# Kernel optimization log

Measured on AMD Instinct MI355X. Metric: run time of the kernel, lower is better.

## Reference

```python
import jax, jax.numpy as jnp
import numpy as np

EPS = 1e-5
NEG_SLOPE = 0.1


def setup_inputs() -> dict:
    key = jax.random.key(0)
    ks = jax.random.split(key, 4)
    B, Cin, Cout, D, E, EMB = 2, 32, 32, 40, 3, 1
    return {
        "x": jax.random.normal(ks[0], (B, Cin, D, D, D), dtype=jnp.float32),
        "embedding": jax.random.normal(ks[1], (B, EMB), dtype=jnp.float32),
        "route_w": jax.random.normal(ks[2], (EMB, E), dtype=jnp.float32),
        "route_b": jnp.zeros((E,), dtype=jnp.float32),
        "expert_kernels": jax.random.normal(ks[3], (E, Cout, Cin, 3, 3, 3), dtype=jnp.float32) * 0.05,
        "expert_bias": jnp.zeros((E, Cout), dtype=jnp.float32),
        "gamma": jnp.ones((Cout,), dtype=jnp.float32),
        "beta": jnp.zeros((Cout,), dtype=jnp.float32),
    }


def reference(x, embedding, route_w, route_b, expert_kernels, expert_bias, gamma, beta):
    # CondConv routing: sigmoid(Linear(embedding)) -> per-sample expert weights [B, E]
    r = jax.nn.sigmoid(embedding @ route_w + route_b)
    # Per-sample combined kernel [B, O, I, 3, 3, 3] and bias [B, O]
    w = jnp.einsum('be,eoixyz->boixyz', r, expert_kernels)
    b = r @ expert_bias

    def conv_one(xi, wi):
        # xi: [Cin, D, H, W], wi: [O, I, 3, 3, 3] -> [Cout, D, H, W]
        return jax.lax.conv_general_dilated(
            xi[None], wi, window_strides=(1, 1, 1), padding='SAME',
            dimension_numbers=('NCDHW', 'OIDHW', 'NCDHW'))[0]

    y = jax.vmap(conv_one)(x, w) + b[:, :, None, None, None]  # [B, O, D, H, W]

    # BatchNorm3d (training mode: biased batch stats over B,D,H,W per channel)
    mean = jnp.mean(y, axis=(0, 2, 3, 4), keepdims=True)
    var = jnp.mean(jnp.square(y - mean), axis=(0, 2, 3, 4), keepdims=True)
    y = (y - mean) * jax.lax.rsqrt(var + EPS)
    y = y * gamma[None, :, None, None, None] + beta[None, :, None, None, None]

    # LeakyReLU(0.1)
    y = jnp.where(y >= 0, y, NEG_SLOPE * y)

    # Upsample nearest, scale_factor=2 on all 3 spatial dims
    y = jnp.repeat(jnp.repeat(jnp.repeat(y, 2, axis=2), 2, axis=3), 2, axis=4)
    return y
```

## Files before the change

### kernel.cpp

```cpp
#include <hip/hip_runtime.h>
#include <hip/hip_bf16.h>
#include <math.h>

#define BB   2
#define CIN  32
#define COUT 32
#define DM   40
#define PD   42
#define NPTS (DM*DM)
#define NVOL (DM*DM*DM)
#define EPSBN 1e-5f
#define NSLOT 64

typedef short  bf16x8  __attribute__((ext_vector_type(8)));
typedef float  floatx4 __attribute__((ext_vector_type(4)));

#define WS_WFRAG 0
#define WS_BCOMB 27648
#define WS_SUM2  27712
#define WS_XPAD2 31808
#define WS_Y     2402624

#define REPACK_BLOCKS (PD*PD*BB)
#define NW_ELEMS  (2*2*27*64*8)
#define PREP_ELEMS (NW_ELEMS + 64 + NSLOT*64)
#define PREP_BLOCKS ((PREP_ELEMS + 255) / 256)

__global__ void prep_repack_kernel(const float* __restrict__ x,
                                   const float* __restrict__ emb,
                                   const float* __restrict__ rw,
                                   const float* __restrict__ rb,
                                   const float* __restrict__ ek,
                                   const float* __restrict__ ebias,
                                   float* __restrict__ ws) {
    const int bid = blockIdx.x;
    if (bid < REPACK_BLOCKS) {
        int b  = bid / (PD * PD);
        int r  = bid % (PD * PD);
        int zp = r / PD, yp = r % PD;
        __hip_bfloat16* row = (__hip_bfloat16*)(ws + WS_XPAD2) +
                              ((((size_t)b * PD + zp) * PD + yp) * PD) * 32;
        bool inz = (zp >= 1 && zp <= DM && yp >= 1 && yp <= DM);
        for (int idx = threadIdx.x; idx < PD * 32; idx += 256) {
            int i = idx & 31, xp = idx >> 5;
            float v = 0.0f;
            if (inz && xp >= 1 && xp <= DM)
                v = x[(size_t)(b * CIN + i) * NVOL +
                      (zp - 1) * NPTS + (yp - 1) * DM + (xp - 1)];
            row[idx] = __float2bfloat16(v);
        }
        return;
    }
    int idx = (bid - REPACK_BLOCKS) * 256 + threadIdx.x;
    __hip_bfloat16* wfrag = (__hip_bfloat16*)(ws + WS_WFRAG);
    if (idx < NW_ELEMS) {
        int j    = idx & 7;
        int lane = (idx >> 3) & 63;
        int tap  = (idx >> 9) % 27;
        int nt   = (idx / (27 * 512)) & 1;
        int b    = idx / (2 * 27 * 512);
        int o = nt * 16 + (lane & 15);
        int i = (lane >> 4) * 8 + j;
        float e0 = emb[b];
        float w = 0.0f;
        #pragma unroll
        for (int e = 0; e < 3; ++e) {
            float r = 1.0f / (1.0f + expf(-(e0 * rw[e] + rb[e])));
            w += r * ek[((e * COUT + o) * CIN + i) * 27 + tap];
        }
        wfrag[idx] = __float2bfloat16(w);
    } else if (idx < NW_ELEMS + 64) {
        int j2 = idx - NW_ELEMS;
        int b = j2 >> 5, o = j2 & 31;
        float e0 = emb[b];
        float bv = 0.0f;
        #pragma unroll
        for (int e = 0; e < 3; ++e) {
            float r = 1.0f / (1.0f + expf(-(e0 * rw[e] + rb[e])));
            bv += r * ebias[e * COUT + o];
        }
        ws[WS_BCOMB + j2] = bv;
    } else if (idx < PREP_ELEMS) {
        ws[WS_SUM2 + (idx - NW_ELEMS - 64)] = 0.0f;
    }
}

__global__ __launch_bounds__(256, 4) void conv_mfma_kernel(
        const __hip_bfloat16* __restrict__ xp2,
        const bf16x8* __restrict__ wfrag,
        const float* __restrict__ bcomb,
        float* __restrict__ y,
        float* __restrict__ sums2) {
    const int mc = blockIdx.x, z = blockIdx.y, b = blockIdx.z;
    const int tid = threadIdx.x, lane = tid & 63, wv = tid >> 6;
    const int mt = wv & 1, nt = wv >> 1;
    const int quad = lane >> 4, l15 = lane & 15;

    __shared__ float lstat[64];
    if (tid < 64) lstat[tid] = 0.0f;
    __syncthreads();

    const int pa = mc * 32 + mt * 16 + l15;
    const int ya = pa / DM, xa = pa % DM;
    const char* abase = (const char*)xp2 +
        ((((size_t)b * PD + z) * PD + ya) * PD + xa) * 64 + quad * 16;
    const bf16x8* wbase = wfrag + ((b * 2 + nt) * 27) * 64 + lane;

    floatx4 acc0 = {0.f, 0.f, 0.f, 0.f};
    floatx4 acc1 = {0.f, 0.f, 0.f, 0.f};
    #pragma unroll
    for (int t = 0; t < 27; ++t) {
        const int dz = t / 9, dy = (t / 3) % 3, dx = t % 3;
        bf16x8 av = *(const bf16x8*)(abase + ((dz * PD + dy) * PD + dx) * 64);
        bf16x8 bv = wbase[t * 64];
        if (t & 1) acc1 = __builtin_amdgcn_mfma_f32_16x16x32_bf16(av, bv, acc1, 0, 0, 0);
        else       acc0 = __builtin_amdgcn_mfma_f32_16x16x32_bf16(av, bv, acc0, 0, 0, 0);
    }
    floatx4 acc = acc0 + acc1;

    const int o = nt * 16 + l15;
    const float bias = bcomb[b * COUT + o];
    const int po = mc * 32 + mt * 16 + quad * 4;
    float v0 = acc[0] + bias;
    float v1 = acc[1] + bias;
    float v2 = acc[2] + bias;
    float v3 = acc[3] + bias;
    *(float4*)(y + ((size_t)(b * COUT + o) * DM + z) * NPTS + po) =
        make_float4(v0, v1, v2, v3);

    float vs = v0 + v1 + v2 + v3;
    float vq = v0 * v0 + v1 * v1 + v2 * v2 + v3 * v3;
    vs += __shfl_xor(vs, 16); vq += __shfl_xor(vq, 16);
    vs += __shfl_xor(vs, 32); vq += __shfl_xor(vq, 32);
    if (lane < 16) {
        atomicAdd(&lstat[o],      vs);
        atomicAdd(&lstat[32 + o], vq);
    }
    __syncthreads();
    if (tid < 64) {
        int slot = ((b * DM + z) * 50 + mc) & (NSLOT - 1);
        atomicAdd(&sums2[slot * 64 + tid], lstat[tid]);
    }
}

__global__ void upsample_kernel(const float* __restrict__ yin,
                                const float* __restrict__ sums2,
                                const float* __restrict__ gamma,
                                const float* __restrict__ beta,
                                float* __restrict__ out) {
    __shared__ float partl[4][64];
    __shared__ float ssc[32], ssh[32];
    const int tid = threadIdx.x;
    {
        int sg = tid >> 6, st = tid & 63;
        float p = 0.0f;
        #pragma unroll
        for (int s = 0; s < 16; ++s) p += sums2[(sg * 16 + s) * 64 + st];
        partl[sg][st] = p;
    }
    __syncthreads();
    if (tid < 64) {
        partl[0][tid] += partl[1][tid] + partl[2][tid] + partl[3][tid];
    }
    __syncthreads();
    if (tid < 32) {
        const float invN = 1.0f / (float)(BB * NVOL);
        float mean  = partl[0][tid] * invN;
        float var   = partl[0][32 + tid] * invN - mean * mean;
        float scale = gamma[tid] * rsqrtf(var + EPSBN);
        ssc[tid] = scale;
        ssh[tid] = beta[tid] - mean * scale;
    }
    __syncthreads();

    int idx = blockIdx.x * 256 + tid;
    int cc = idx / (NVOL / 2);
    int p  = idx % (NVOL / 2);
    int z  = p / (NPTS / 2);
    int yy = (p / (DM / 2)) % DM;
    int x2 = p % (DM / 2);
    int c  = cc & 31;

    float2 v = *(const float2*)(yin + (size_t)idx * 2);
    float sc = ssc[c], sh = ssh[c];
    float w0 = v.x * sc + sh; w0 = (w0 >= 0.0f) ? w0 : 0.1f * w0;
    float w1 = v.y * sc + sh; w1 = (w1 >= 0.0f) ? w1 : 0.1f * w1;

    float4 q = make_float4(w0, w0, w1, w1);
    size_t obase = ((size_t)cc * 80 + (size_t)(2 * z)) * 6400
                 + (size_t)(2 * yy) * 80 + (size_t)(4 * x2);
    *(float4*)(out + obase)        = q;
    *(float4*)(out + obase + 80)   = q;
    *(float4*)(out + obase + 6400) = q;
    *(float4*)(out + obase + 6480) = q;
}

extern "C" void kernel_launch(void* const* d_in, const int* in_sizes, int n_in,
                              void* d_out, int out_size, void* d_ws, size_t ws_size,
                              hipStream_t stream) {
    const float* x     = (const float*)d_in[0];
    const float* emb   = (const float*)d_in[1];
    const float* rw    = (const float*)d_in[2];
    const float* rb    = (const float*)d_in[3];
    const float* ek    = (const float*)d_in[4];
    const float* ebias = (const float*)d_in[5];
    const float* gamma = (const float*)d_in[6];
    const float* beta  = (const float*)d_in[7];
    float* ws  = (float*)d_ws;
    float* out = (float*)d_out;

    prep_repack_kernel<<<REPACK_BLOCKS + PREP_BLOCKS, 256, 0, stream>>>(
        x, emb, rw, rb, ek, ebias, ws);

    conv_mfma_kernel<<<dim3(50, DM, BB), 256, 0, stream>>>(
        (const __hip_bfloat16*)(ws + WS_XPAD2), (const bf16x8*)(ws + WS_WFRAG),
        ws + WS_BCOMB, ws + WS_Y, ws + WS_SUM2);

    upsample_kernel<<<(BB * COUT * NVOL / 2) / 256, 256, 0, stream>>>(
        ws + WS_Y, ws + WS_SUM2, gamma, beta, out);
}
```

Measured before the change: 206.0 us.

## Store conv intermediate as bf16, double per-wave M tile, nontemporal upsample stores

The conv kernel now computes two 16-point M tiles per wave, reusing each weight fragment across both, and halves its grid. The pre-norm activation is written as bf16 instead of fp32, which halves the intermediate write and read traffic. The upsample kernel reads four bf16 values per thread and writes the 8x-expanded output with nontemporal stores. BN statistics are still accumulated from the fp32 values, but the stored activations lose precision before normalisation.

```diff
diff --git a/kernel.cpp b/kernel.cpp
--- a/kernel.cpp
+++ b/kernel.cpp
@@ -13,6 +13,7 @@
 #define NSLOT 64
 
 typedef short  bf16x8  __attribute__((ext_vector_type(8)));
+typedef short  bf16x4  __attribute__((ext_vector_type(4)));
 typedef float  floatx4 __attribute__((ext_vector_type(4)));
 
 #define WS_WFRAG 0
@@ -25,6 +26,16 @@
 #define NW_ELEMS  (2*2*27*64*8)
 #define PREP_ELEMS (NW_ELEMS + 64 + NSLOT*64)
 #define PREP_BLOCKS ((PREP_ELEMS + 255) / 256)
+
+static __device__ __forceinline__ short f2bf(float f) {
+    __hip_bfloat16 h = __float2bfloat16(f);
+    return *reinterpret_cast<short*>(&h);
+}
+static __device__ __forceinline__ float bf2f(short s) {
+    union { unsigned u; float f; } cv;
+    cv.u = ((unsigned)(unsigned short)s) << 16;
+    return cv.f;
+}
 
 __global__ void prep_repack_kernel(const float* __restrict__ x,
                                    const float* __restrict__ emb,
@@ -89,7 +100,7 @@
         const __hip_bfloat16* __restrict__ xp2,
         const bf16x8* __restrict__ wfrag,
         const float* __restrict__ bcomb,
-        float* __restrict__ y,
+        __hip_bfloat16* __restrict__ y,
         float* __restrict__ sums2) {
     const int mc = blockIdx.x, z = blockIdx.y, b = blockIdx.z;
     const int tid = threadIdx.x, lane = tid & 63, wv = tid >> 6;
@@ -100,10 +111,14 @@
     if (tid < 64) lstat[tid] = 0.0f;
     __syncthreads();
 
-    const int pa = mc * 32 + mt * 16 + l15;
-    const int ya = pa / DM, xa = pa % DM;
-    const char* abase = (const char*)xp2 +
-        ((((size_t)b * PD + z) * PD + ya) * PD + xa) * 64 + quad * 16;
+    const int pa0 = mc * 64 + mt * 32 + l15;
+    const int pa1 = pa0 + 16;
+    const int ya0 = pa0 / DM, xa0 = pa0 % DM;
+    const int ya1 = pa1 / DM, xa1 = pa1 % DM;
+    const char* abase0 = (const char*)xp2 +
+        ((((size_t)b * PD + z) * PD + ya0) * PD + xa0) * 64 + quad * 16;
+    const char* abase1 = (const char*)xp2 +
+        ((((size_t)b * PD + z) * PD + ya1) * PD + xa1) * 64 + quad * 16;
     const bf16x8* wbase = wfrag + ((b * 2 + nt) * 27) * 64 + lane;
 
     floatx4 acc0 = {0.f, 0.f, 0.f, 0.f};
@@ -111,25 +126,32 @@
     #pragma unroll
     for (int t = 0; t < 27; ++t) {
         const int dz = t / 9, dy = (t / 3) % 3, dx = t % 3;
-        bf16x8 av = *(const bf16x8*)(abase + ((dz * PD + dy) * PD + dx) * 64);
-        bf16x8 bv = wbase[t * 64];
-        if (t & 1) acc1 = __builtin_amdgcn_mfma_f32_16x16x32_bf16(av, bv, acc1, 0, 0, 0);
-        else       acc0 = __builtin_amdgcn_mfma_f32_16x16x32_bf16(av, bv, acc0, 0, 0, 0);
-    }
-    floatx4 acc = acc0 + acc1;
+        const int aoff = ((dz * PD + dy) * PD + dx) * 64;
+        bf16x8 av0 = *(const bf16x8*)(abase0 + aoff);
+        bf16x8 av1 = *(const bf16x8*)(abase1 + aoff);
+        bf16x8 bv  = wbase[t * 64];
+        acc0 = __builtin_amdgcn_mfma_f32_16x16x32_bf16(av0, bv, acc0, 0, 0, 0);
+        acc1 = __builtin_amdgcn_mfma_f32_16x16x32_bf16(av1, bv, acc1, 0, 0, 0);
+    }
 
     const int o = nt * 16 + l15;
     const float bias = bcomb[b * COUT + o];
-    const int po = mc * 32 + mt * 16 + quad * 4;
-    float v0 = acc[0] + bias;
-    float v1 = acc[1] + bias;
-    float v2 = acc[2] + bias;
-    float v3 = acc[3] + bias;
-    *(float4*)(y + ((size_t)(b * COUT + o) * DM + z) * NPTS + po) =
-        make_float4(v0, v1, v2, v3);
-
-    float vs = v0 + v1 + v2 + v3;
-    float vq = v0 * v0 + v1 * v1 + v2 * v2 + v3 * v3;
+    const int po0 = mc * 64 + mt * 32 + quad * 4;
+    const int po1 = po0 + 16;
+
+    float u0 = acc0[0] + bias, u1 = acc0[1] + bias;
+    float u2 = acc0[2] + bias, u3 = acc0[3] + bias;
+    float w0 = acc1[0] + bias, w1 = acc1[1] + bias;
+    float w2 = acc1[2] + bias, w3 = acc1[3] + bias;
+
+    __hip_bfloat16* yrow = y + ((size_t)(b * COUT + o) * DM + z) * NPTS;
+    bf16x4 p0 = { f2bf(u0), f2bf(u1), f2bf(u2), f2bf(u3) };
+    bf16x4 p1 = { f2bf(w0), f2bf(w1), f2bf(w2), f2bf(w3) };
+    *(bf16x4*)(yrow + po0) = p0;
+    *(bf16x4*)(yrow + po1) = p1;
+
+    float vs = u0 + u1 + u2 + u3 + w0 + w1 + w2 + w3;
+    float vq = u0*u0 + u1*u1 + u2*u2 + u3*u3 + w0*w0 + w1*w1 + w2*w2 + w3*w3;
     vs += __shfl_xor(vs, 16); vq += __shfl_xor(vq, 16);
     vs += __shfl_xor(vs, 32); vq += __shfl_xor(vq, 32);
     if (lane < 16) {
@@ -138,12 +160,12 @@
     }
     __syncthreads();
     if (tid < 64) {
-        int slot = ((b * DM + z) * 50 + mc) & (NSLOT - 1);
+        int slot = ((b * DM + z) * 25 + mc) & (NSLOT - 1);
         atomicAdd(&sums2[slot * 64 + tid], lstat[tid]);
     }
 }
 
-__global__ void upsample_kernel(const float* __restrict__ yin,
+__global__ void upsample_kernel(const __hip_bfloat16* __restrict__ yin,
                                 const float* __restrict__ sums2,
                                 const float* __restrict__ gamma,
                                 const float* __restrict__ beta,
@@ -174,25 +196,32 @@
     __syncthreads();
 
     int idx = blockIdx.x * 256 + tid;
-    int cc = idx / (NVOL / 2);
-    int p  = idx % (NVOL / 2);
-    int z  = p / (NPTS / 2);
-    int yy = (p / (DM / 2)) % DM;
-    int x2 = p % (DM / 2);
+    int cc = idx / (NVOL / 4);
+    int p  = idx % (NVOL / 4);
+    int z  = p / (NPTS / 4);
+    int yy = (p / (DM / 4)) % DM;
+    int x4 = p % (DM / 4);
     int c  = cc & 31;
 
-    float2 v = *(const float2*)(yin + (size_t)idx * 2);
+    bf16x4 rv = *(const bf16x4*)(yin + (size_t)idx * 4);
     float sc = ssc[c], sh = ssh[c];
-    float w0 = v.x * sc + sh; w0 = (w0 >= 0.0f) ? w0 : 0.1f * w0;
-    float w1 = v.y * sc + sh; w1 = (w1 >= 0.0f) ? w1 : 0.1f * w1;
-
-    float4 q = make_float4(w0, w0, w1, w1);
+    float v0 = bf2f(rv[0]) * sc + sh; v0 = (v0 >= 0.0f) ? v0 : 0.1f * v0;
+    float v1 = bf2f(rv[1]) * sc + sh; v1 = (v1 >= 0.0f) ? v1 : 0.1f * v1;
+    float v2 = bf2f(rv[2]) * sc + sh; v2 = (v2 >= 0.0f) ? v2 : 0.1f * v2;
+    float v3 = bf2f(rv[3]) * sc + sh; v3 = (v3 >= 0.0f) ? v3 : 0.1f * v3;
+
+    floatx4 q01 = {v0, v0, v1, v1};
+    floatx4 q23 = {v2, v2, v3, v3};
     size_t obase = ((size_t)cc * 80 + (size_t)(2 * z)) * 6400
-                 + (size_t)(2 * yy) * 80 + (size_t)(4 * x2);
-    *(float4*)(out + obase)        = q;
-    *(float4*)(out + obase + 80)   = q;
-    *(float4*)(out + obase + 6400) = q;
-    *(float4*)(out + obase + 6480) = q;
+                 + (size_t)(2 * yy) * 80 + (size_t)(8 * x4);
+    __builtin_nontemporal_store(q01, (floatx4*)(out + obase));
+    __builtin_nontemporal_store(q23, (floatx4*)(out + obase + 4));
+    __builtin_nontemporal_store(q01, (floatx4*)(out + obase + 80));
+    __builtin_nontemporal_store(q23, (floatx4*)(out + obase + 84));
+    __builtin_nontemporal_store(q01, (floatx4*)(out + obase + 6400));
+    __builtin_nontemporal_store(q23, (floatx4*)(out + obase + 6404));
+    __builtin_nontemporal_store(q01, (floatx4*)(out + obase + 6480));
+    __builtin_nontemporal_store(q23, (floatx4*)(out + obase + 6484));
 }
 
 extern "C" void kernel_launch(void* const* d_in, const int* in_sizes, int n_in,
@@ -212,10 +241,10 @@
     prep_repack_kernel<<<REPACK_BLOCKS + PREP_BLOCKS, 256, 0, stream>>>(
         x, emb, rw, rb, ek, ebias, ws);
 
-    conv_mfma_kernel<<<dim3(50, DM, BB), 256, 0, stream>>>(
+    conv_mfma_kernel<<<dim3(25, DM, BB), 256, 0, stream>>>(
         (const __hip_bfloat16*)(ws + WS_XPAD2), (const bf16x8*)(ws + WS_WFRAG),
-        ws + WS_BCOMB, ws + WS_Y, ws + WS_SUM2);
-
-    upsample_kernel<<<(BB * COUT * NVOL / 2) / 256, 256, 0, stream>>>(
-        ws + WS_Y, ws + WS_SUM2, gamma, beta, out);
-}
+        ws + WS_BCOMB, (__hip_bfloat16*)(ws + WS_Y), ws + WS_SUM2);
+
+    upsample_kernel<<<(BB * COUT * NVOL / 4) / 256, 256, 0, stream>>>(
+        (const __hip_bfloat16*)(ws + WS_Y), ws + WS_SUM2, gamma, beta, out);
+}
```

New measurement: 234.9 us. 14.1% more time.
